# Kernel optimization log

Measured on AMD Instinct MI355X. Metric: run time of the kernel, lower is better.

## Reference

```python
import jax, jax.numpy as jnp
import numpy as np

NODE_TYPES = ('user', 'vn', 'tag', 'staff', 'producer', 'character', 'trait')
N = {'user': 100000, 'vn': 40000, 'tag': 3000, 'staff': 20000, 'producer': 8000, 'character': 60000, 'trait': 3000}
# (src_type, dst_type) per edge type, in HGATConfig.edge_types order
EDGE_TYPES = (('user','vn'), ('vn','user'), ('vn','tag'), ('tag','vn'), ('vn','staff'), ('staff','vn'),
              ('vn','staff'), ('staff','vn'), ('vn','producer'), ('producer','vn'), ('vn','character'),
              ('character','vn'), ('character','trait'), ('trait','character'))
E_COUNTS = (1000000, 1000000, 500000, 500000, 200000, 200000, 200000, 200000, 100000, 100000, 300000, 300000, 400000, 400000)
HID = 128
LAYERS = 3
# number of edge types targeting each node type (HeteroConv aggr='mean' divisor)
NUM_DST = {'user': 1, 'vn': 6, 'tag': 1, 'staff': 2, 'producer': 1, 'character': 2, 'trait': 1}


def _l2norm(x):
    n = jnp.linalg.norm(x, axis=-1, keepdims=True)
    return x / jnp.maximum(n, 1e-12)


def _layernorm(x, g, b):
    m = jnp.mean(x, axis=-1, keepdims=True)
    v = jnp.mean((x - m) ** 2, axis=-1, keepdims=True)
    return (x - m) * jax.lax.rsqrt(v + 1e-5) * g + b


def _forward(xs, Wp, bp, Wl, bl, Wr, ln_g, ln_b, Wu, bu, Wv, bv, eis):
    # input projection per node type
    h = {t: xs[t] @ Wp[i].T + bp[i] for i, t in enumerate(NODE_TYPES)}
    # inverse in-degree per edge type (constant across layers)
    inv_deg = []
    for e, (st, dt) in enumerate(EDGE_TYPES):
        dst = eis[e][1]
        deg = jax.ops.segment_sum(jnp.ones(dst.shape[0], jnp.float32), dst, num_segments=N[dt])
        inv_deg.append(1.0 / jnp.maximum(deg, 1.0))
    for l in range(LAYERS):
        acc = {t: jnp.zeros((N[t], HID), h[t].dtype) for t in NODE_TYPES}
        for e, (st, dt) in enumerate(EDGE_TYPES):
            src, dst = eis[e][0], eis[e][1]
            # SAGEConv: mean-aggregate neighbor feats, then lin_l(agg) + lin_r(root), L2-normalize
            agg = jax.ops.segment_sum(h[st][src], dst, num_segments=N[dt]) * inv_deg[e][:, None]
            out = agg @ Wl[l, e].T + bl[l, e] + h[dt] @ Wr[l, e].T
            acc[dt] = acc[dt] + _l2norm(out)
        new_h = {}
        for i, t in enumerate(NODE_TYPES):
            x = acc[t] / NUM_DST[t] + h[t]  # HeteroConv mean over edge types + residual
            new_h[t] = jax.nn.relu(_layernorm(x, ln_g[l, i], ln_b[l, i]))  # dropout = identity (eval)
        h = new_h
    user_emb = _l2norm(h['user'] @ Wu.T + bu)
    vn_emb = _l2norm(h['vn'] @ Wv.T + bv)
    return user_emb, vn_emb


def setup_inputs() -> dict:
    key = jax.random.key(0)
    ks = iter(jax.random.split(key, 80))
    inp = {}
    for t in NODE_TYPES:
        inp['x_' + t] = jax.random.normal(next(ks), (N[t], HID), jnp.float32)
    for e, (st, dt) in enumerate(EDGE_TYPES):
        src = jax.random.randint(next(ks), (E_COUNTS[e],), 0, N[st], jnp.int32)
        dst = jax.random.randint(next(ks), (E_COUNTS[e],), 0, N[dt], jnp.int32)
        inp['ei_%d' % e] = jnp.stack([src, dst])
    s = 1.0 / np.sqrt(HID)
    inp['Wp'] = jax.random.normal(next(ks), (7, HID, HID), jnp.float32) * s
    inp['bp'] = jnp.zeros((7, HID), jnp.float32)
    inp['Wl'] = jax.random.normal(next(ks), (LAYERS, 14, HID, HID), jnp.float32) * s
    inp['bl'] = jnp.zeros((LAYERS, 14, HID), jnp.float32)
    inp['Wr'] = jax.random.normal(next(ks), (LAYERS, 14, HID, HID), jnp.float32) * s
    inp['ln_g'] = jnp.ones((LAYERS, 7, HID), jnp.float32)
    inp['ln_b'] = jnp.zeros((LAYERS, 7, HID), jnp.float32)
    inp['Wu'] = jax.random.normal(next(ks), (HID, HID), jnp.float32) * s
    inp['bu'] = jnp.zeros((HID,), jnp.float32)
    inp['Wv'] = jax.random.normal(next(ks), (HID, HID), jnp.float32) * s
    inp['bv'] = jnp.zeros((HID,), jnp.float32)
    return inp


def reference(x_user, x_vn, x_tag, x_staff, x_producer, x_character, x_trait,
              ei_0, ei_1, ei_2, ei_3, ei_4, ei_5, ei_6, ei_7, ei_8, ei_9, ei_10, ei_11, ei_12, ei_13,
              Wp, bp, Wl, bl, Wr, ln_g, ln_b, Wu, bu, Wv, bv):
    xs = {'user': x_user, 'vn': x_vn, 'tag': x_tag, 'staff': x_staff,
          'producer': x_producer, 'character': x_character, 'trait': x_trait}
    eis = [ei_0, ei_1, ei_2, ei_3, ei_4, ei_5, ei_6, ei_7, ei_8, ei_9, ei_10, ei_11, ei_12, ei_13]
    return _forward(xs, Wp, bp, Wl, bl, Wr, ln_g, ln_b, Wu, bu, Wv, bv, eis)
```

## Files before the change

### kernel.cpp

```cpp
#include <hip/hip_runtime.h>
#include <math.h>

#define TOTE 5400000
#define TOTN 234000
#define TOTC 514000
#define HID  128

#define NBUK 499
#define NBLK 1024


typedef __attribute__((ext_vector_type(8))) short short8;
typedef __attribute__((ext_vector_type(8))) __bf16 bf16x8;
typedef __attribute__((ext_vector_type(4))) float floatx4;
typedef __attribute__((ext_vector_type(2))) float float2v;

__constant__ int c_EPRE[15]   = {0,1000000,2000000,2500000,3000000,3200000,3400000,3600000,3800000,3900000,4000000,4300000,4600000,5000000,5400000};
__constant__ int c_ECNT[14]   = {1000000,1000000,500000,500000,200000,200000,200000,200000,100000,100000,300000,300000,400000,400000};
__constant__ int c_CNTOFF[14] = {0,40000,140000,143000,183000,203000,243000,263000,303000,311000,351000,411000,451000,454000};
__constant__ int c_CNTN[14]   = {40000,100000,3000,40000,20000,40000,20000,40000,8000,40000,60000,40000,3000,60000};
__constant__ int c_SRCOFF[14] = {0,100000,100000,140000,100000,143000,100000,143000,100000,163000,100000,171000,171000,231000};
__constant__ int c_NODEPRE[8] = {0,100000,140000,143000,163000,171000,231000,234000};
__constant__ float c_INVND[7] = {1.0f, 1.0f/6.0f, 1.0f, 0.5f, 1.0f, 0.5f, 1.0f};
__constant__ int c_UPD_NS[7]      = {1,6,1,2,1,2,1};
__constant__ int c_UPD_BASE[7][6] = {
    {40000,0,0,0,0,0},
    {0,143000,203000,263000,311000,411000},
    {140000,0,0,0,0,0},
    {183000,243000,0,0,0,0},
    {303000,0,0,0,0,0},
    {351000,454000,0,0,0,0},
    {451000,0,0,0,0,0}};
__constant__ int c_BSH[14]   = {9,10,6,10,10,11,10,11,10,11,11,11,6,11};
__constant__ int c_BBASE[15] = {0,79,177,224,264,284,304,324,344,352,372,402,422,469,499};

static __device__ __forceinline__ unsigned short f2bf(float f) {
    unsigned u = __float_as_uint(f);
    u = u + 0x7FFFu + ((u >> 16) & 1u);
    return (unsigned short)(u >> 16);
}
static __device__ __forceinline__ float bf2f(unsigned short s) {
    return __uint_as_float(((unsigned)s) << 16);
}
static __device__ __forceinline__ unsigned short f2h(float f) {
    _Float16 h = (_Float16)f;
    return __builtin_bit_cast(unsigned short, h);
}
static __device__ __forceinline__ float h2f(unsigned short s) {
    _Float16 h = __builtin_bit_cast(_Float16, s);
    return (float)h;
}

struct EdgeArgs { const int* ei[14]; };


__global__ __launch_bounds__(256) void hist_k(EdgeArgs a, int* __restrict__ blkHist) {
    __shared__ int h[NBUK];
    int t = threadIdx.x;
    for (int i = t; i < NBUK; i += 256) h[i] = 0;
    __syncthreads();
    const int per = (TOTE + NBLK - 1) / NBLK;
    int s = blockIdx.x * per;
    int eEnd = min(s + per, TOTE);
    for (int g = s + t; g < eEnd; g += 256) {
        int e = 0;
        while (g >= c_EPRE[e + 1]) e++;
        int k = g - c_EPRE[e];
        int dst = a.ei[e][c_ECNT[e] + k];
        atomicAdd(&h[c_BBASE[e] + (dst >> c_BSH[e])], 1);
    }
    __syncthreads();
    for (int i = t; i < NBUK; i += 256) blkHist[(size_t)i * NBLK + blockIdx.x] = h[i];
}

__global__ __launch_bounds__(256) void scan_blk_k(int* __restrict__ blkHist, int* __restrict__ bktCnt) {
    int b = blockIdx.x;
    int* p = blkHist + (size_t)b * NBLK;
    int t = threadIdx.x;
    int4 v = *(int4*)&p[t * 4];
    int s = v.x + v.y + v.z + v.w;
    int lane = t & 63, w = t >> 6;
    __shared__ int wt[4];
    int incl = s;
    #pragma unroll
    for (int d = 1; d < 64; d <<= 1) { int o = __shfl_up(incl, d); if (lane >= d) incl += o; }
    if (lane == 63) wt[w] = incl;
    __syncthreads();
    int wb = 0;
    for (int i = 0; i < w; i++) wb += wt[i];
    int excl = incl - s + wb;
    int4 o;
    o.x = excl; o.y = excl + v.x; o.z = excl + v.x + v.y; o.w = excl + v.x + v.y + v.z;
    *(int4*)&p[t * 4] = o;
    if (t == 255) bktCnt[b] = excl + s;
}

__global__ __launch_bounds__(512) void scans2_k(const int* __restrict__ bktCnt, int* __restrict__ bktEdgeBase) {
    int t = threadIdx.x;
    int v = (t < NBUK) ? bktCnt[t] : 0;
    int lane = t & 63, w = t >> 6;
    __shared__ int wt[8];
    int incl = v;
    #pragma unroll
    for (int d = 1; d < 64; d <<= 1) { int o = __shfl_up(incl, d); if (lane >= d) incl += o; }
    if (lane == 63) wt[w] = incl;
    __syncthreads();
    int wb = 0;
    for (int i = 0; i < w; i++) wb += wt[i];
    int excl = incl - v + wb;
    if (t < NBUK) bktEdgeBase[t] = excl;
    if (t == NBUK - 1) bktEdgeBase[NBUK] = excl + v;
}

__global__ __launch_bounds__(256) void scatter_k(EdgeArgs a, const int* __restrict__ blkHist,
        const int* __restrict__ bktEdgeBase, unsigned* __restrict__ pool) {
    __shared__ int cur[NBUK];
    int t = threadIdx.x;
    for (int i = t; i < NBUK; i += 256)
        cur[i] = bktEdgeBase[i] + blkHist[(size_t)i * NBLK + blockIdx.x];
    __syncthreads();
    const int per = (TOTE + NBLK - 1) / NBLK;
    int s = blockIdx.x * per;
    int eEnd = min(s + per, TOTE);
    for (int g = s + t; g < eEnd; g += 256) {
        int e = 0;
        while (g >= c_EPRE[e + 1]) e++;
        int k = g - c_EPRE[e];
        int src = a.ei[e][k];
        int dst = a.ei[e][c_ECNT[e] + k];
        int sh = c_BSH[e];
        unsigned rec = ((unsigned)(dst & ((1 << sh) - 1)) << 18) | (unsigned)(c_SRCOFF[e] + src);
        int p = atomicAdd(&cur[c_BBASE[e] + (dst >> sh)], 1);
        pool[p] = rec;
    }
}

__global__ __launch_bounds__(256) void csrfill_k(
        const unsigned* __restrict__ pool, const int* __restrict__ bktEdgeBase,
        int* __restrict__ cnt, int* __restrict__ cursor, float* __restrict__ invdeg,
        int* __restrict__ col) {
    __shared__ int hist[2048];
    __shared__ int cur[2048];
    __shared__ int wtot[4];
    __shared__ int wbase[4];
    int b = blockIdx.x;
    int t = threadIdx.x;
    int e = 0;
    while (b >= c_BBASE[e + 1]) e++;
    int lb = b - c_BBASE[e];
    int sh = c_BSH[e];
    int s0t = lb << sh;
    int span = min(1 << sh, c_CNTN[e] - s0t);
    int gs0 = c_CNTOFF[e] + s0t;
    int ebase = bktEdgeBase[b];
    int nrec = bktEdgeBase[b + 1] - ebase;

    for (int i = t; i < span; i += 256) hist[i] = 0;
    __syncthreads();
    for (int i = t; i < nrec; i += 256) atomicAdd(&hist[pool[ebase + i] >> 18], 1);
    __syncthreads();
    int base = t * 8, loc = 0, lv[8];
    #pragma unroll
    for (int i = 0; i < 8; i++) {
        int ii = base + i;
        int v = (ii < span) ? hist[ii] : 0;
        lv[i] = loc; loc += v;
    }
    int lane = t & 63, w = t >> 6;
    int incl = loc;
    #pragma unroll
    for (int d = 1; d < 64; d <<= 1) { int o = __shfl_up(incl, d); if (lane >= d) incl += o; }
    if (lane == 63) wtot[w] = incl;
    __syncthreads();
    if (t == 0) { int s2 = 0; for (int i = 0; i < 4; i++) { wbase[i] = s2; s2 += wtot[i]; } }
    __syncthreads();
    int texcl = incl - loc + wbase[w];
    #pragma unroll
    for (int i = 0; i < 8; i++) {
        int ii = base + i;
        if (ii < span) cur[ii] = texcl + lv[i];
    }
    __syncthreads();
    for (int i = t; i < span; i += 256) {
        int c = hist[i];
        cnt[gs0 + i] = c;
        cursor[gs0 + i] = ebase + cur[i] + c;
        invdeg[gs0 + i] = 1.0f / fmaxf((float)c, 1.0f);
    }
    __syncthreads();
    for (int i = t; i < nrec; i += 256) {
        unsigned rec = pool[ebase + i];
        int p = atomicAdd(&cur[rec >> 18], 1);
        col[ebase + p] = (int)(rec & 0x3FFFFu);
    }
}

struct XArgs { const float* x[7]; };
__global__ __launch_bounds__(256) void convx_k(XArgs a, unsigned short* __restrict__ hbf) {
    int i4 = blockIdx.x * 256 + threadIdx.x;
    if (i4 >= TOTN * 32) return;
    int idx = i4 * 4;
    int t = 0;
    while (idx >= c_NODEPRE[t + 1] * 128) t++;
    float4 v = *(const float4*)&a.x[t][idx - c_NODEPRE[t] * 128];
    uint2 p;
    p.x = (unsigned)f2bf(v.x) | ((unsigned)f2bf(v.y) << 16);
    p.y = (unsigned)f2bf(v.z) | ((unsigned)f2bf(v.w) << 16);
    *(uint2*)&hbf[idx] = p;
}

struct WArgs { const float* Wp; const float* Wl; const float* Wr; const float* Wu; const float* Wv; };
__global__ __launch_bounds__(256) void convw_k(WArgs a, unsigned short* __restrict__ wbf) {
    int i4 = blockIdx.x * 256 + threadIdx.x;
    if (i4 >= 93 * 4096) return;
    int idx = i4 * 4;
    int m = idx >> 14;
    int i = idx & 16383;
    const float* src;
    if (m < 7)       src = a.Wp + (size_t)m * 16384;
    else if (m < 49) src = a.Wl + (size_t)(m - 7) * 16384;
    else if (m < 91) src = a.Wr + (size_t)(m - 49) * 16384;
    else if (m == 91) src = a.Wu;
    else              src = a.Wv;
    float4 v = *(const float4*)&src[i];
    uint2 p;
    p.x = (unsigned)f2bf(v.x) | ((unsigned)f2bf(v.y) << 16);
    p.y = (unsigned)f2bf(v.z) | ((unsigned)f2bf(v.w) << 16);
    *(uint2*)&wbf[idx] = p;
}

#define ACC8v(u) do { \
    v01 += (float2v){__uint_as_float((u).x << 16), __uint_as_float((u).x & 0xFFFF0000u)}; \
    v23 += (float2v){__uint_as_float((u).y << 16), __uint_as_float((u).y & 0xFFFF0000u)}; \
    v45 += (float2v){__uint_as_float((u).z << 16), __uint_as_float((u).z & 0xFFFF0000u)}; \
    v67 += (float2v){__uint_as_float((u).w << 16), __uint_as_float((u).w & 0xFFFF0000u)}; } while (0)

__global__ __launch_bounds__(256) void agg_k(
        const int* __restrict__ cnt, const int* __restrict__ cursor,
        const float* __restrict__ inv_deg, const int* __restrict__ col,
        const unsigned short* __restrict__ hbf, unsigned short* __restrict__ slotb) {
    int row = blockIdx.x * 4 + (threadIdx.x >> 6);
    if (row >= TOTC) return;
    int lane = threadIdx.x & 63;
    int q = lane >> 4, li = lane & 15;
    int nn = cnt[row];
    int rs = cursor[row] - nn;
    const int* cp = col + rs;
    float2v v01 = {0.f, 0.f}, v23 = {0.f, 0.f}, v45 = {0.f, 0.f}, v67 = {0.f, 0.f};
    int j = 0;
    if (j + 8 <= nn) {
        int c0 = cp[q], c1 = cp[4 + q];
        for (; j + 8 <= nn; ) {
            int jn = j + 8;
            int n0 = 0, n1 = 0;
            if (jn + 8 <= nn) { n0 = cp[jn + q]; n1 = cp[jn + 4 + q]; }
            uint4 u0 = *(const uint4*)&hbf[(c0 << 7) + li * 8];
            uint4 u1 = *(const uint4*)&hbf[(c1 << 7) + li * 8];
            ACC8v(u0);
            ACC8v(u1);
            c0 = n0; c1 = n1; j = jn;
        }
    }
    for (; j < nn; j += 4) {
        if (j + q < nn) {
            int c = cp[j + q] << 7;
            uint4 u = *(const uint4*)&hbf[c + li * 8];
            ACC8v(u);
        }
    }
    float inv = inv_deg[row];
    float v[8] = {v01.x, v01.y, v23.x, v23.y, v45.x, v45.y, v67.x, v67.y};
    #pragma unroll
    for (int i = 0; i < 8; i++) {
        v[i] += __shfl_xor(v[i], 16);
        v[i] += __shfl_xor(v[i], 32);
        v[i] *= inv;
    }
    if (q == 0) {
        uint4 o;
        o.x = (unsigned)f2bf(v[0]) | ((unsigned)f2bf(v[1]) << 16);
        o.y = (unsigned)f2bf(v[2]) | ((unsigned)f2bf(v[3]) << 16);
        o.z = (unsigned)f2bf(v[4]) | ((unsigned)f2bf(v[5]) << 16);
        o.w = (unsigned)f2bf(v[6]) | ((unsigned)f2bf(v[7]) << 16);
        *(uint4*)&slotb[(size_t)row * HID + li * 8] = o;
    }
}

struct GemmLArgs {
    int blockPrefix[15];
    const unsigned short* W1[14];
    const unsigned short* W2[14];
    const float* bias[14];
    int cntoff[14];
    int dstoff[14];
    int rows[14];
};

__global__ __launch_bounds__(256) void gemm_l(GemmLArgs g,
        const unsigned short* __restrict__ hbf, unsigned short* __restrict__ slotb) {
    __shared__ short A1s[128 * 40];
    __shared__ short A2s[128 * 40];
    __shared__ short W1s[128 * 40];
    __shared__ short W2s[128 * 40];
    int b = blockIdx.x;
    int s = 0;
    while (b >= g.blockPrefix[s + 1]) s++;
    int rows = g.rows[s];
    int row0 = (b - g.blockPrefix[s]) * 128;
    int t = threadIdx.x;
    int wv = t >> 6, lane = t & 63;
    int q = lane >> 4, m15 = lane & 15;

    const uint4* A14 = (const uint4*)(slotb + (size_t)g.cntoff[s] * HID);
    const uint4* A24 = (const uint4*)(hbf + (size_t)g.dstoff[s] * HID);
    const uint4* W14 = (const uint4*)g.W1[s];
    const uint4* W24 = (const uint4*)g.W2[s];

    floatx4 acc[2][8];
    #pragma unroll
    for (int m = 0; m < 2; m++)
        #pragma unroll
        for (int bb = 0; bb < 8; bb++) acc[m][bb] = (floatx4){0.f, 0.f, 0.f, 0.f};

    for (int k0 = 0; k0 < 4; k0++) {
        __syncthreads();
        #pragma unroll
        for (int i = 0; i < 2; i++) {
            int idx = t + i * 256;
            int row = idx >> 2, kc = idx & 3;
            uint4 va1 = make_uint4(0u, 0u, 0u, 0u), va2 = va1;
            if (row0 + row < rows) {
                va1 = A14[(size_t)(row0 + row) * 16 + k0 * 4 + kc];
                va2 = A24[(size_t)(row0 + row) * 16 + k0 * 4 + kc];
            }
            *(uint4*)&A1s[row * 40 + kc * 8] = va1;
            *(uint4*)&A2s[row * 40 + kc * 8] = va2;
            uint4 w1 = W14[(size_t)row * 16 + k0 * 4 + kc];
            uint4 w2 = W24[(size_t)row * 16 + k0 * 4 + kc];
            *(uint4*)&W1s[row * 40 + kc * 8] = w1;
            *(uint4*)&W2s[row * 40 + kc * 8] = w2;
        }
        __syncthreads();
        bf16x8 a1[2], a2[2];
        #pragma unroll
        for (int m = 0; m < 2; m++) {
            int r = (wv * 32 + m * 16 + m15) * 40 + q * 8;
            a1[m] = __builtin_bit_cast(bf16x8, *(const short8*)&A1s[r]);
            a2[m] = __builtin_bit_cast(bf16x8, *(const short8*)&A2s[r]);
        }
        #pragma unroll
        for (int bb = 0; bb < 8; bb++) {
            int r = (bb * 16 + m15) * 40 + q * 8;
            bf16x8 w1 = __builtin_bit_cast(bf16x8, *(const short8*)&W1s[r]);
            bf16x8 w2 = __builtin_bit_cast(bf16x8, *(const short8*)&W2s[r]);
            #pragma unroll
            for (int m = 0; m < 2; m++) {
                acc[m][bb] = __builtin_amdgcn_mfma_f32_16x16x32_bf16(a1[m], w1, acc[m][bb], 0, 0, 0);
                acc[m][bb] = __builtin_amdgcn_mfma_f32_16x16x32_bf16(a2[m], w2, acc[m][bb], 0, 0, 0);
            }
        }
    }

    const float* bias = g.bias[s];
    #pragma unroll
    for (int bb = 0; bb < 8; bb++) {
        float bv = bias[bb * 16 + m15];
        #pragma unroll
        for (int m = 0; m < 2; m++)
            #pragma unroll
            for (int reg = 0; reg < 4; reg++) acc[m][bb][reg] += bv;
    }
    unsigned short* outp = slotb + (size_t)g.cntoff[s] * HID;
    #pragma unroll
    for (int m = 0; m < 2; m++) {
        #pragma unroll
        for (int reg = 0; reg < 4; reg++) {
            float ss = 0.f;
            #pragma unroll
            for (int bb = 0; bb < 8; bb++) ss += acc[m][bb][reg] * acc[m][bb][reg];
            ss += __shfl_xor(ss, 1);
            ss += __shfl_xor(ss, 2);
            ss += __shfl_xor(ss, 4);
            ss += __shfl_xor(ss, 8);
            float sc = 1.0f / fmaxf(sqrtf(ss), 1e-12f);
            int r = row0 + wv * 32 + m * 16 + q * 4 + reg;
            if (r < rows) {
                unsigned short* o = outp + (size_t)r * HID;
                #pragma unroll
                for (int bb = 0; bb < 8; bb++)
                    o[bb * 16 + m15] = f2h(acc[m][bb][reg] * sc);
            }
        }
    }
}

struct GemmArgs {
    int blockPrefix[15];
    const unsigned short* A1[14];
    const unsigned short* W1[14];
    const float* bias[14]; void* out[14];
    int rows[14];
};

template<int MODE>
__global__ __launch_bounds__(256) void gemm_k(GemmArgs g) {
    __shared__ short As[64 * 40];
    __shared__ short Ws[128 * 40];
    int b = blockIdx.x;
    int s = 0;
    while (b >= g.blockPrefix[s + 1]) s++;
    int rows = g.rows[s];
    int row0 = (b - g.blockPrefix[s]) * 64;
    int t = threadIdx.x;
    int w = t >> 6, lane = t & 63;
    int q = lane >> 4, m15 = lane & 15;

    floatx4 acc[8];
    #pragma unroll
    for (int bb = 0; bb < 8; bb++) acc[bb] = (floatx4){0.f, 0.f, 0.f, 0.f};

    const uint4* A4 = (const uint4*)g.A1[s];
    const uint4* W4 = (const uint4*)g.W1[s];
    for (int k0 = 0; k0 < 128; k0 += 32) {
        __syncthreads();
        {
            int row = t >> 2, kc = t & 3;
            uint4 v = make_uint4(0u, 0u, 0u, 0u);
            if (row0 + row < rows) v = A4[(size_t)(row0 + row) * 16 + (k0 >> 3) + kc];
            *(uint4*)&As[row * 40 + kc * 8] = v;
        }
        #pragma unroll
        for (int i = 0; i < 2; i++) {
            int idx = t + i * 256;
            int c = idx >> 2, kc = idx & 3;
            uint4 v = W4[(size_t)c * 16 + (k0 >> 3) + kc];
            *(uint4*)&Ws[c * 40 + kc * 8] = v;
        }
        __syncthreads();
        bf16x8 af = __builtin_bit_cast(bf16x8, *(const short8*)&As[(w * 16 + m15) * 40 + q * 8]);
        #pragma unroll
        for (int bb = 0; bb < 8; bb++) {
            bf16x8 bf = __builtin_bit_cast(bf16x8, *(const short8*)&Ws[(bb * 16 + m15) * 40 + q * 8]);
            acc[bb] = __builtin_amdgcn_mfma_f32_16x16x32_bf16(af, bf, acc[bb], 0, 0, 0);
        }
    }

    const float* bias = g.bias[s];
    #pragma unroll
    for (int bb = 0; bb < 8; bb++) {
        float bv = bias[bb * 16 + m15];
        #pragma unroll
        for (int reg = 0; reg < 4; reg++) acc[bb][reg] += bv;
    }
    if (MODE != 0) {
        #pragma unroll
        for (int reg = 0; reg < 4; reg++) {
            float ss = 0.f;
            #pragma unroll
            for (int bb = 0; bb < 8; bb++) ss += acc[bb][reg] * acc[bb][reg];
            ss += __shfl_xor(ss, 1);
            ss += __shfl_xor(ss, 2);
            ss += __shfl_xor(ss, 4);
            ss += __shfl_xor(ss, 8);
            float sc = 1.0f / fmaxf(sqrtf(ss), 1e-12f);
            #pragma unroll
            for (int bb = 0; bb < 8; bb++) acc[bb][reg] *= sc;
        }
    }
    int rbase = row0 + w * 16 + q * 4;
    if (MODE == 3) {
        float* out = (float*)g.out[s];
        #pragma unroll
        for (int reg = 0; reg < 4; reg++) {
            int r = rbase + reg;
            if (r < rows) {
                float* o = out + (size_t)r * HID;
                #pragma unroll
                for (int bb = 0; bb < 8; bb++) o[bb * 16 + m15] = acc[bb][reg];
            }
        }
    } else {
        unsigned short* out = (unsigned short*)g.out[s];
        #pragma unroll
        for (int reg = 0; reg < 4; reg++) {
            int r = rbase + reg;
            if (r < rows) {
                unsigned short* o = out + (size_t)r * HID;
                #pragma unroll
                for (int bb = 0; bb < 8; bb++) o[bb * 16 + m15] = f2bf(acc[bb][reg]);
            }
        }
    }
}

__global__ __launch_bounds__(256) void update_k(unsigned short* __restrict__ hbf,
                                                const unsigned short* __restrict__ slotb,
                                                const float* __restrict__ ln_g, const float* __restrict__ ln_b, int l) {
    int row = blockIdx.x * 4 + (threadIdx.x >> 6);
    if (row >= TOTN) return;
    int lane = threadIdx.x & 63;
    int t = 0;
    while (row >= c_NODEPRE[t + 1]) t++;
    int r = row - c_NODEPRE[t];
    int ns = c_UPD_NS[t];
    float s0 = 0.f, s1 = 0.f;
    for (int s = 0; s < ns; s++) {
        const unsigned short* sp = slotb + (size_t)(c_UPD_BASE[t][s] + r) * HID;
        s0 += h2f(sp[lane]);
        s1 += h2f(sp[lane + 64]);
    }
    float invnd = c_INVND[t];
    const float* gg = ln_g + ((size_t)l * 7 + t) * HID;
    const float* bb = ln_b + ((size_t)l * 7 + t) * HID;
    unsigned short* hp = hbf + (size_t)row * HID;
    float x0 = s0 * invnd + bf2f(hp[lane]);
    float x1 = s1 * invnd + bf2f(hp[lane + 64]);
    float s = x0 + x1;
    s += __shfl_xor(s, 1);  s += __shfl_xor(s, 2);  s += __shfl_xor(s, 4);
    s += __shfl_xor(s, 8);  s += __shfl_xor(s, 16); s += __shfl_xor(s, 32);
    float mean = s * (1.0f / 128.0f);
    float d0 = x0 - mean, d1 = x1 - mean;
    float vs = d0 * d0 + d1 * d1;
    vs += __shfl_xor(vs, 1);  vs += __shfl_xor(vs, 2);  vs += __shfl_xor(vs, 4);
    vs += __shfl_xor(vs, 8);  vs += __shfl_xor(vs, 16); vs += __shfl_xor(vs, 32);
    float rstd = rsqrtf(vs * (1.0f / 128.0f) + 1e-5f);
    float y0 = d0 * rstd * gg[lane]      + bb[lane];
    float y1 = d1 * rstd * gg[lane + 64] + bb[lane + 64];
    hp[lane]      = f2bf(fmaxf(y0, 0.f));
    hp[lane + 64] = f2bf(fmaxf(y1, 0.f));
}

extern "C" void kernel_launch(void* const* d_in, const int* in_sizes, int n_in,
                              void* d_out, int out_size, void* d_ws, size_t ws_size,
                              hipStream_t stream) {
    (void)in_sizes; (void)n_in; (void)out_size; (void)ws_size;
    const float* Wp   = (const float*)d_in[21];
    const float* bp   = (const float*)d_in[22];
    const float* Wl   = (const float*)d_in[23];
    const float* bl   = (const float*)d_in[24];
    const float* Wr   = (const float*)d_in[25];
    const float* ln_g = (const float*)d_in[26];
    const float* ln_b = (const float*)d_in[27];
    const float* Wu   = (const float*)d_in[28];
    const float* bu   = (const float*)d_in[29];
    const float* Wv   = (const float*)d_in[30];
    const float* bv   = (const float*)d_in[31];
    float* out = (float*)d_out;

    unsigned short* h_bf   = (unsigned short*)d_ws;
    unsigned short* w_bf   = h_bf + (size_t)TOTN * HID;
    unsigned short* slotb  = w_bf + (size_t)93 * 16384;
    int*            cnt    = (int*)(slotb + (size_t)TOTC * HID);
    int*            cursor = cnt + TOTC;
    float*          invdeg = (float*)(cursor + TOTC);
    unsigned*       pool   = (unsigned*)(invdeg + TOTC);
    int*            blkHist = (int*)(pool + (size_t)TOTE);
    int*            ctrl    = blkHist + (size_t)NBUK * NBLK;
    int* bktCnt       = ctrl;
    int* bktEdgeBase  = ctrl + NBUK;

    int* col = (int*)d_out;

    static const int CNTOFF[14] = {0,40000,140000,143000,183000,203000,243000,263000,303000,311000,351000,411000,451000,454000};
    static const int CNTN[14]   = {40000,100000,3000,40000,20000,40000,20000,40000,8000,40000,60000,40000,3000,60000};
    static const int DSTOFF[14] = {100000,0,140000,100000,143000,100000,143000,100000,163000,100000,171000,100000,231000,171000};
    static const int NODEPRE[8] = {0,100000,140000,143000,163000,171000,231000,234000};
    static const int NT[7]      = {100000,40000,3000,20000,8000,60000,3000};

    EdgeArgs ea;
    for (int e = 0; e < 14; e++) ea.ei[e] = (const int*)d_in[7 + e];

    hist_k<<<NBLK, 256, 0, stream>>>(ea, blkHist);
    scan_blk_k<<<NBUK, 256, 0, stream>>>(blkHist, bktCnt);
    scans2_k<<<1, 512, 0, stream>>>(bktCnt, bktEdgeBase);
    scatter_k<<<NBLK, 256, 0, stream>>>(ea, blkHist, bktEdgeBase, pool);
    csrfill_k<<<NBUK, 256, 0, stream>>>(pool, bktEdgeBase, cnt, cursor, invdeg, col);

    {
        XArgs xa;
        for (int t = 0; t < 7; t++) xa.x[t] = (const float*)d_in[t];
        convx_k<<<(TOTN * 32 + 255) / 256, 256, 0, stream>>>(xa, h_bf);
        WArgs wa = {Wp, Wl, Wr, Wu, Wv};
        convw_k<<<(93 * 4096 + 255) / 256, 256, 0, stream>>>(wa, w_bf);
    }

    {
        GemmArgs ga;
        int pre = 0; ga.blockPrefix[0] = 0;
        for (int t = 0; t < 7; t++) {
            ga.A1[t] = h_bf + (size_t)NODEPRE[t] * HID;
            ga.W1[t] = w_bf + (size_t)t * 16384;
            ga.bias[t] = bp + (size_t)t * HID;
            ga.out[t] = h_bf + (size_t)NODEPRE[t] * HID;
            ga.rows[t] = NT[t];
            pre += (NT[t] + 63) / 64;
            ga.blockPrefix[t + 1] = pre;
        }
        for (int s = 7; s < 14; s++) { ga.blockPrefix[s + 1] = pre; ga.rows[s] = 0; }
        gemm_k<0><<<pre, 256, 0, stream>>>(ga);
    }

    int lgrid;
    GemmLArgs gl;
    {
        int pre = 0; gl.blockPrefix[0] = 0;
        for (int e = 0; e < 14; e++) {
            gl.rows[e]   = CNTN[e];
            gl.cntoff[e] = CNTOFF[e];
            gl.dstoff[e] = DSTOFF[e];
            pre += (CNTN[e] + 127) / 128;
            gl.blockPrefix[e + 1] = pre;
        }
        lgrid = pre;
    }
    for (int l = 0; l < 3; l++) {
        agg_k<<<(TOTC + 3) / 4, 256, 0, stream>>>(cnt, cursor, invdeg, col, h_bf, slotb);
        for (int e = 0; e < 14; e++) {
            gl.W1[e]   = w_bf + (size_t)(7  + l * 14 + e) * 16384;
            gl.W2[e]   = w_bf + (size_t)(49 + l * 14 + e) * 16384;
            gl.bias[e] = bl + ((size_t)l * 14 + e) * HID;
        }
        gemm_l<<<lgrid, 256, 0, stream>>>(gl, h_bf, slotb);
        update_k<<<(TOTN + 3) / 4, 256, 0, stream>>>(h_bf, slotb, ln_g, ln_b, l);
    }

    {
        GemmArgs ga;
        ga.blockPrefix[0] = 0;
        ga.A1[0] = h_bf;
        ga.W1[0] = w_bf + (size_t)91 * 16384;
        ga.bias[0] = bu;                        ga.out[0] = out;
        ga.rows[0] = 100000;
        ga.blockPrefix[1] = (100000 + 63) / 64;
        ga.A1[1] = h_bf + (size_t)100000 * HID;
        ga.W1[1] = w_bf + (size_t)92 * 16384;
        ga.bias[1] = bv;                        ga.out[1] = out + (size_t)100000 * HID;
        ga.rows[1] = 40000;
        int tot = ga.blockPrefix[1] + (40000 + 63) / 64;
        for (int s = 2; s < 14; s++) { ga.blockPrefix[s + 1] = tot; ga.rows[s] = 0; }
        ga.blockPrefix[2] = tot;
        gemm_k<3><<<tot, 256, 0, stream>>>(ga);
    }
}
```

Baseline: 1.598 ms.

## Fuse per-edge-type SAGE GEMM with hetero-mean, residual and LayerNorm update

Replaces the per-edge-type gemm_l kernel, which wrote L2-normalized fp16 outputs back to the slot buffer, and the separate update_k kernel with a single kernel per destination node type. Each 64-row block loops over the edge types feeding its node type, keeps the dst root features resident in LDS, accumulates the normalized outputs in registers, then applies the mean over edge types, the residual, LayerNorm and ReLU, and writes bf16 h. This removes the slot write/read round trip and one launch per layer. In exchange, blocks shrink from 128 to 64 rows, which lowers weight reuse per block, and vn blocks do six times more work than others, which can cause load imbalance.

```diff
diff --git a/kernel.cpp b/kernel.cpp
--- a/kernel.cpp
+++ b/kernel.cpp
@@ -21,16 +21,6 @@
 __constant__ int c_CNTN[14]   = {40000,100000,3000,40000,20000,40000,20000,40000,8000,40000,60000,40000,3000,60000};
 __constant__ int c_SRCOFF[14] = {0,100000,100000,140000,100000,143000,100000,143000,100000,163000,100000,171000,171000,231000};
 __constant__ int c_NODEPRE[8] = {0,100000,140000,143000,163000,171000,231000,234000};
-__constant__ float c_INVND[7] = {1.0f, 1.0f/6.0f, 1.0f, 0.5f, 1.0f, 0.5f, 1.0f};
-__constant__ int c_UPD_NS[7]      = {1,6,1,2,1,2,1};
-__constant__ int c_UPD_BASE[7][6] = {
-    {40000,0,0,0,0,0},
-    {0,143000,203000,263000,311000,411000},
-    {140000,0,0,0,0,0},
-    {183000,243000,0,0,0,0},
-    {303000,0,0,0,0,0},
-    {351000,454000,0,0,0,0},
-    {451000,0,0,0,0,0}};
 __constant__ int c_BSH[14]   = {9,10,6,10,10,11,10,11,10,11,11,11,6,11};
 __constant__ int c_BBASE[15] = {0,79,177,224,264,284,304,324,344,352,372,402,422,469,499};
 
@@ -41,14 +31,6 @@
 }
 static __device__ __forceinline__ float bf2f(unsigned short s) {
     return __uint_as_float(((unsigned)s) << 16);
-}
-static __device__ __forceinline__ unsigned short f2h(float f) {
-    _Float16 h = (_Float16)f;
-    return __builtin_bit_cast(unsigned short, h);
-}
-static __device__ __forceinline__ float h2f(unsigned short s) {
-    _Float16 h = __builtin_bit_cast(_Float16, s);
-    return (float)h;
 }
 
 struct EdgeArgs { const int* ei[14]; };
@@ -286,109 +268,147 @@
     }
 }
 
-struct GemmLArgs {
-    int blockPrefix[15];
-    const unsigned short* W1[14];
-    const unsigned short* W2[14];
-    const float* bias[14];
-    int cntoff[14];
-    int dstoff[14];
-    int rows[14];
+struct FusArgs {
+    int blockPrefix[8];
+    int ns[7];
+    int a1off[7][6];
+    const unsigned short* W1[7][6];
+    const unsigned short* W2[7][6];
+    const float* bias[7][6];
+    int nodepre[7];
+    int nrows[7];
+    float invnd[7];
 };
 
-__global__ __launch_bounds__(256) void gemm_l(GemmLArgs g,
-        const unsigned short* __restrict__ hbf, unsigned short* __restrict__ slotb) {
-    __shared__ short A1s[128 * 40];
-    __shared__ short A2s[128 * 40];
-    __shared__ short W1s[128 * 40];
-    __shared__ short W2s[128 * 40];
+__global__ __launch_bounds__(256) void fusedln_k(FusArgs g,
+        unsigned short* __restrict__ hbf, const unsigned short* __restrict__ slotb,
+        const float* __restrict__ ln_g, const float* __restrict__ ln_b, int l) {
+    __shared__ short As2[64 * 168];
+    __shared__ short A1c[64 * 40];
+    __shared__ short W1c[128 * 40];
+    __shared__ short W2c[128 * 40];
     int b = blockIdx.x;
-    int s = 0;
-    while (b >= g.blockPrefix[s + 1]) s++;
-    int rows = g.rows[s];
-    int row0 = (b - g.blockPrefix[s]) * 128;
-    int t = threadIdx.x;
-    int wv = t >> 6, lane = t & 63;
+    int t = 0;
+    while (b >= g.blockPrefix[t + 1]) t++;
+    int nrows = g.nrows[t];
+    int row0 = (b - g.blockPrefix[t]) * 64;
+    int dst0 = g.nodepre[t] + row0;
+    int tid = threadIdx.x;
+    int w = tid >> 6, lane = tid & 63;
     int q = lane >> 4, m15 = lane & 15;
 
-    const uint4* A14 = (const uint4*)(slotb + (size_t)g.cntoff[s] * HID);
-    const uint4* A24 = (const uint4*)(hbf + (size_t)g.dstoff[s] * HID);
-    const uint4* W14 = (const uint4*)g.W1[s];
-    const uint4* W24 = (const uint4*)g.W2[s];
-
-    floatx4 acc[2][8];
-    #pragma unroll
-    for (int m = 0; m < 2; m++)
-        #pragma unroll
-        for (int bb = 0; bb < 8; bb++) acc[m][bb] = (floatx4){0.f, 0.f, 0.f, 0.f};
-
-    for (int k0 = 0; k0 < 4; k0++) {
-        __syncthreads();
-        #pragma unroll
-        for (int i = 0; i < 2; i++) {
-            int idx = t + i * 256;
-            int row = idx >> 2, kc = idx & 3;
-            uint4 va1 = make_uint4(0u, 0u, 0u, 0u), va2 = va1;
-            if (row0 + row < rows) {
-                va1 = A14[(size_t)(row0 + row) * 16 + k0 * 4 + kc];
-                va2 = A24[(size_t)(row0 + row) * 16 + k0 * 4 + kc];
+    {
+        const uint4* h4 = (const uint4*)hbf;
+        #pragma unroll
+        for (int it = 0; it < 4; it++) {
+            int c = tid + it * 256;
+            int row = c >> 4, kc = c & 15;
+            uint4 v = make_uint4(0u, 0u, 0u, 0u);
+            if (row0 + row < nrows) v = h4[(size_t)(dst0 + row) * 16 + kc];
+            *(uint4*)&As2[row * 168 + (kc >> 2) * 40 + (kc & 3) * 8] = v;
+        }
+    }
+
+    floatx4 accsum[8];
+    #pragma unroll
+    for (int bb = 0; bb < 8; bb++) accsum[bb] = (floatx4){0.f, 0.f, 0.f, 0.f};
+
+    int ns = g.ns[t];
+    for (int ei = 0; ei < ns; ei++) {
+        const uint4* A14 = (const uint4*)(slotb + (size_t)g.a1off[t][ei] * HID);
+        const uint4* W14 = (const uint4*)g.W1[t][ei];
+        const uint4* W24 = (const uint4*)g.W2[t][ei];
+        floatx4 acc[8];
+        #pragma unroll
+        for (int bb = 0; bb < 8; bb++) acc[bb] = (floatx4){0.f, 0.f, 0.f, 0.f};
+        for (int k0 = 0; k0 < 4; k0++) {
+            __syncthreads();
+            {
+                int row = tid >> 2, kc = tid & 3;
+                uint4 v = make_uint4(0u, 0u, 0u, 0u);
+                if (row0 + row < nrows) v = A14[(size_t)(row0 + row) * 16 + k0 * 4 + kc];
+                *(uint4*)&A1c[row * 40 + kc * 8] = v;
             }
-            *(uint4*)&A1s[row * 40 + kc * 8] = va1;
-            *(uint4*)&A2s[row * 40 + kc * 8] = va2;
-            uint4 w1 = W14[(size_t)row * 16 + k0 * 4 + kc];
-            uint4 w2 = W24[(size_t)row * 16 + k0 * 4 + kc];
-            *(uint4*)&W1s[row * 40 + kc * 8] = w1;
-            *(uint4*)&W2s[row * 40 + kc * 8] = w2;
-        }
-        __syncthreads();
-        bf16x8 a1[2], a2[2];
-        #pragma unroll
-        for (int m = 0; m < 2; m++) {
-            int r = (wv * 32 + m * 16 + m15) * 40 + q * 8;
-            a1[m] = __builtin_bit_cast(bf16x8, *(const short8*)&A1s[r]);
-            a2[m] = __builtin_bit_cast(bf16x8, *(const short8*)&A2s[r]);
-        }
+            #pragma unroll
+            for (int i = 0; i < 2; i++) {
+                int idx = tid + i * 256;
+                int c = idx >> 2, kc = idx & 3;
+                *(uint4*)&W1c[c * 40 + kc * 8] = W14[(size_t)c * 16 + k0 * 4 + kc];
+                *(uint4*)&W2c[c * 40 + kc * 8] = W24[(size_t)c * 16 + k0 * 4 + kc];
+            }
+            __syncthreads();
+            bf16x8 a1 = __builtin_bit_cast(bf16x8, *(const short8*)&A1c[(w * 16 + m15) * 40 + q * 8]);
+            bf16x8 a2 = __builtin_bit_cast(bf16x8, *(const short8*)&As2[(w * 16 + m15) * 168 + k0 * 40 + q * 8]);
+            #pragma unroll
+            for (int bb = 0; bb < 8; bb++) {
+                bf16x8 w1 = __builtin_bit_cast(bf16x8, *(const short8*)&W1c[(bb * 16 + m15) * 40 + q * 8]);
+                bf16x8 w2 = __builtin_bit_cast(bf16x8, *(const short8*)&W2c[(bb * 16 + m15) * 40 + q * 8]);
+                acc[bb] = __builtin_amdgcn_mfma_f32_16x16x32_bf16(a1, w1, acc[bb], 0, 0, 0);
+                acc[bb] = __builtin_amdgcn_mfma_f32_16x16x32_bf16(a2, w2, acc[bb], 0, 0, 0);
+            }
+        }
+        const float* bias = g.bias[t][ei];
         #pragma unroll
         for (int bb = 0; bb < 8; bb++) {
-            int r = (bb * 16 + m15) * 40 + q * 8;
-            bf16x8 w1 = __builtin_bit_cast(bf16x8, *(const short8*)&W1s[r]);
-            bf16x8 w2 = __builtin_bit_cast(bf16x8, *(const short8*)&W2s[r]);
-            #pragma unroll
-            for (int m = 0; m < 2; m++) {
-                acc[m][bb] = __builtin_amdgcn_mfma_f32_16x16x32_bf16(a1[m], w1, acc[m][bb], 0, 0, 0);
-                acc[m][bb] = __builtin_amdgcn_mfma_f32_16x16x32_bf16(a2[m], w2, acc[m][bb], 0, 0, 0);
-            }
-        }
-    }
-
-    const float* bias = g.bias[s];
-    #pragma unroll
-    for (int bb = 0; bb < 8; bb++) {
-        float bv = bias[bb * 16 + m15];
-        #pragma unroll
-        for (int m = 0; m < 2; m++)
-            #pragma unroll
-            for (int reg = 0; reg < 4; reg++) acc[m][bb][reg] += bv;
-    }
-    unsigned short* outp = slotb + (size_t)g.cntoff[s] * HID;
-    #pragma unroll
-    for (int m = 0; m < 2; m++) {
+            float bv = bias[bb * 16 + m15];
+            #pragma unroll
+            for (int reg = 0; reg < 4; reg++) acc[bb][reg] += bv;
+        }
         #pragma unroll
         for (int reg = 0; reg < 4; reg++) {
             float ss = 0.f;
             #pragma unroll
-            for (int bb = 0; bb < 8; bb++) ss += acc[m][bb][reg] * acc[m][bb][reg];
+            for (int bb = 0; bb < 8; bb++) ss += acc[bb][reg] * acc[bb][reg];
             ss += __shfl_xor(ss, 1);
             ss += __shfl_xor(ss, 2);
             ss += __shfl_xor(ss, 4);
             ss += __shfl_xor(ss, 8);
             float sc = 1.0f / fmaxf(sqrtf(ss), 1e-12f);
-            int r = row0 + wv * 32 + m * 16 + q * 4 + reg;
-            if (r < rows) {
-                unsigned short* o = outp + (size_t)r * HID;
-                #pragma unroll
-                for (int bb = 0; bb < 8; bb++)
-                    o[bb * 16 + m15] = f2h(acc[m][bb][reg] * sc);
+            #pragma unroll
+            for (int bb = 0; bb < 8; bb++) accsum[bb][reg] += acc[bb][reg] * sc;
+        }
+    }
+
+    float invnd = g.invnd[t];
+    const float* gg = ln_g + ((size_t)l * 7 + t) * HID;
+    const float* bbp = ln_b + ((size_t)l * 7 + t) * HID;
+    float gv[8], bv2[8];
+    #pragma unroll
+    for (int bb = 0; bb < 8; bb++) {
+        gv[bb]  = gg[bb * 16 + m15];
+        bv2[bb] = bbp[bb * 16 + m15];
+    }
+    #pragma unroll
+    for (int reg = 0; reg < 4; reg++) {
+        int lrow = w * 16 + q * 4 + reg;
+        float x[8];
+        #pragma unroll
+        for (int bb = 0; bb < 8; bb++) {
+            float resid = bf2f((unsigned short)As2[lrow * 168 + (bb >> 1) * 40 + (bb & 1) * 16 + m15]);
+            x[bb] = accsum[bb][reg] * invnd + resid;
+        }
+        float s = 0.f;
+        #pragma unroll
+        for (int bb = 0; bb < 8; bb++) s += x[bb];
+        s += __shfl_xor(s, 1);
+        s += __shfl_xor(s, 2);
+        s += __shfl_xor(s, 4);
+        s += __shfl_xor(s, 8);
+        float mean = s * (1.0f / 128.0f);
+        float vs = 0.f;
+        #pragma unroll
+        for (int bb = 0; bb < 8; bb++) { float d = x[bb] - mean; vs += d * d; }
+        vs += __shfl_xor(vs, 1);
+        vs += __shfl_xor(vs, 2);
+        vs += __shfl_xor(vs, 4);
+        vs += __shfl_xor(vs, 8);
+        float rstd = rsqrtf(vs * (1.0f / 128.0f) + 1e-5f);
+        if (row0 + lrow < nrows) {
+            unsigned short* o = hbf + (size_t)(dst0 + lrow) * HID;
+            #pragma unroll
+            for (int bb = 0; bb < 8; bb++) {
+                float y = (x[bb] - mean) * rstd * gv[bb] + bv2[bb];
+                o[bb * 16 + m15] = f2bf(fmaxf(y, 0.f));
             }
         }
     }
@@ -493,57 +513,16 @@
     }
 }
 
-__global__ __launch_bounds__(256) void update_k(unsigned short* __restrict__ hbf,
-                                                const unsigned short* __restrict__ slotb,
-                                                const float* __restrict__ ln_g, const float* __restrict__ ln_b, int l) {
-    int row = blockIdx.x * 4 + (threadIdx.x >> 6);
-    if (row >= TOTN) return;
-    int lane = threadIdx.x & 63;
-    int t = 0;
-    while (row >= c_NODEPRE[t + 1]) t++;
-    int r = row - c_NODEPRE[t];
-    int ns = c_UPD_NS[t];
-    float s0 = 0.f, s1 = 0.f;
-    for (int s = 0; s < ns; s++) {
-        const unsigned short* sp = slotb + (size_t)(c_UPD_BASE[t][s] + r) * HID;
-        s0 += h2f(sp[lane]);
-        s1 += h2f(sp[lane + 64]);
-    }
-    float invnd = c_INVND[t];
-    const float* gg = ln_g + ((size_t)l * 7 + t) * HID;
-    const float* bb = ln_b + ((size_t)l * 7 + t) * HID;
-    unsigned short* hp = hbf + (size_t)row * HID;
-    float x0 = s0 * invnd + bf2f(hp[lane]);
-    float x1 = s1 * invnd + bf2f(hp[lane + 64]);
-    float s = x0 + x1;
-    s += __shfl_xor(s, 1);  s += __shfl_xor(s, 2);  s += __shfl_xor(s, 4);
-    s += __shfl_xor(s, 8);  s += __shfl_xor(s, 16); s += __shfl_xor(s, 32);
-    float mean = s * (1.0f / 128.0f);
-    float d0 = x0 - mean, d1 = x1 - mean;
-    float vs = d0 * d0 + d1 * d1;
-    vs += __shfl_xor(vs, 1);  vs += __shfl_xor(vs, 2);  vs += __shfl_xor(vs, 4);
-    vs += __shfl_xor(vs, 8);  vs += __shfl_xor(vs, 16); vs += __shfl_xor(vs, 32);
-    float rstd = rsqrtf(vs * (1.0f / 128.0f) + 1e-5f);
-    float y0 = d0 * rstd * gg[lane]      + bb[lane];
-    float y1 = d1 * rstd * gg[lane + 64] + bb[lane + 64];
-    hp[lane]      = f2bf(fmaxf(y0, 0.f));
-    hp[lane + 64] = f2bf(fmaxf(y1, 0.f));
-}
-
 extern "C" void kernel_launch(void* const* d_in, const int* in_sizes, int n_in,
                               void* d_out, int out_size, void* d_ws, size_t ws_size,
                               hipStream_t stream) {
     (void)in_sizes; (void)n_in; (void)out_size; (void)ws_size;
     const float* Wp   = (const float*)d_in[21];
     const float* bp   = (const float*)d_in[22];
-    const float* Wl   = (const float*)d_in[23];
     const float* bl   = (const float*)d_in[24];
-    const float* Wr   = (const float*)d_in[25];
     const float* ln_g = (const float*)d_in[26];
     const float* ln_b = (const float*)d_in[27];
-    const float* Wu   = (const float*)d_in[28];
     const float* bu   = (const float*)d_in[29];
-    const float* Wv   = (const float*)d_in[30];
     const float* bv   = (const float*)d_in[31];
     float* out = (float*)d_out;
 
@@ -562,10 +541,18 @@
     int* col = (int*)d_out;
 
     static const int CNTOFF[14] = {0,40000,140000,143000,183000,203000,243000,263000,303000,311000,351000,411000,451000,454000};
-    static const int CNTN[14]   = {40000,100000,3000,40000,20000,40000,20000,40000,8000,40000,60000,40000,3000,60000};
-    static const int DSTOFF[14] = {100000,0,140000,100000,143000,100000,143000,100000,163000,100000,171000,100000,231000,171000};
     static const int NODEPRE[8] = {0,100000,140000,143000,163000,171000,231000,234000};
     static const int NT[7]      = {100000,40000,3000,20000,8000,60000,3000};
+    static const int FEED_NS[7] = {1,6,1,2,1,2,1};
+    static const int FEED_E[7][6] = {
+        {1,0,0,0,0,0},
+        {0,3,5,7,9,11},
+        {2,0,0,0,0,0},
+        {4,6,0,0,0,0},
+        {8,0,0,0,0,0},
+        {10,13,0,0,0,0},
+        {12,0,0,0,0,0}};
+    static const float INVND[7] = {1.0f, 1.0f/6.0f, 1.0f, 0.5f, 1.0f, 0.5f, 1.0f};
 
     EdgeArgs ea;
     for (int e = 0; e < 14; e++) ea.ei[e] = (const int*)d_in[7 + e];
@@ -580,7 +567,8 @@
         XArgs xa;
         for (int t = 0; t < 7; t++) xa.x[t] = (const float*)d_in[t];
         convx_k<<<(TOTN * 32 + 255) / 256, 256, 0, stream>>>(xa, h_bf);
-        WArgs wa = {Wp, Wl, Wr, Wu, Wv};
+        WArgs wa = {Wp, (const float*)d_in[23], (const float*)d_in[25],
+                    (const float*)d_in[28], (const float*)d_in[30]};
         convw_k<<<(93 * 4096 + 255) / 256, 256, 0, stream>>>(wa, w_bf);
     }
 
@@ -600,28 +588,32 @@
         gemm_k<0><<<pre, 256, 0, stream>>>(ga);
     }
 
-    int lgrid;
-    GemmLArgs gl;
+    FusArgs fa;
+    int fgrid;
     {
-        int pre = 0; gl.blockPrefix[0] = 0;
-        for (int e = 0; e < 14; e++) {
-            gl.rows[e]   = CNTN[e];
-            gl.cntoff[e] = CNTOFF[e];
-            gl.dstoff[e] = DSTOFF[e];
-            pre += (CNTN[e] + 127) / 128;
-            gl.blockPrefix[e + 1] = pre;
-        }
-        lgrid = pre;
+        int pre = 0; fa.blockPrefix[0] = 0;
+        for (int t = 0; t < 7; t++) {
+            fa.ns[t] = FEED_NS[t];
+            fa.nodepre[t] = NODEPRE[t];
+            fa.nrows[t] = NT[t];
+            fa.invnd[t] = INVND[t];
+            for (int j = 0; j < 6; j++) fa.a1off[t][j] = CNTOFF[FEED_E[t][j]];
+            pre += (NT[t] + 63) / 64;
+            fa.blockPrefix[t + 1] = pre;
+        }
+        fgrid = pre;
     }
     for (int l = 0; l < 3; l++) {
         agg_k<<<(TOTC + 3) / 4, 256, 0, stream>>>(cnt, cursor, invdeg, col, h_bf, slotb);
-        for (int e = 0; e < 14; e++) {
-            gl.W1[e]   = w_bf + (size_t)(7  + l * 14 + e) * 16384;
-            gl.W2[e]   = w_bf + (size_t)(49 + l * 14 + e) * 16384;
-            gl.bias[e] = bl + ((size_t)l * 14 + e) * HID;
-        }
-        gemm_l<<<lgrid, 256, 0, stream>>>(gl, h_bf, slotb);
-        update_k<<<(TOTN + 3) / 4, 256, 0, stream>>>(h_bf, slotb, ln_g, ln_b, l);
+        for (int t = 0; t < 7; t++) {
+            for (int j = 0; j < 6; j++) {
+                int e = FEED_E[t][j];
+                fa.W1[t][j]   = w_bf + (size_t)(7  + l * 14 + e) * 16384;
+                fa.W2[t][j]   = w_bf + (size_t)(49 + l * 14 + e) * 16384;
+                fa.bias[t][j] = bl + ((size_t)l * 14 + e) * HID;
+            }
+        }
+        fusedln_k<<<fgrid, 256, 0, stream>>>(fa, h_bf, slotb, ln_g, ln_b, l);
     }
 
     {
```

Measured after the change: 1.500 ms. 1.07x faster.
